# Optimization experiments

Hardware: AMD Instinct MI355X
Metric: run time of the kernel (lower is better)

## Reference

```python
import jax, jax.numpy as jnp
import numpy as np

NUM_NODES = 1_000_000
IN_F, HID_F, OUT_F = 128, 128, 128
N0, N1, T = 16384, 4096, 16


def _safediv(a, b):
    return a / jnp.where(b == 0, jnp.ones_like(b), b)


def _conv(h, nodeset, nb_nodes, nb_w, Qw, Qb, Ww, Wb):
    # gather self + neighbor embeddings (irregular access)
    h_self = h[nodeset]                                   # [n, in]
    h_nb = h[nb_nodes]                                    # [n, T, in]
    q = jax.nn.leaky_relu(jnp.einsum('nti,hi->nth', h_nb, Qw) + Qb)
    agg = _safediv((nb_w[:, :, None] * q).sum(1), nb_w.sum(1, keepdims=True))  # [n, hid]
    h_cat = jnp.concatenate([h_self, agg], axis=1)        # [n, in+hid]
    h_new = jax.nn.leaky_relu(h_cat @ Ww.T + Wb)          # [n, out]
    nrm = jnp.linalg.norm(h_new, axis=1, keepdims=True)
    return _safediv(h_new, nrm)


def setup_inputs() -> dict:
    key = jax.random.key(0)
    ks = jax.random.split(key, 16)
    xav = lambda k, o, i: jax.random.uniform(k, (o, i), jnp.float32, -1.0, 1.0) * jnp.sqrt(6.0 / (o + i)) * jnp.sqrt(2.0)
    return {
        'h': jax.random.normal(ks[0], (NUM_NODES, IN_F), jnp.float32),
        'Qw0': xav(ks[1], HID_F, IN_F), 'Qb0': jnp.zeros((HID_F,), jnp.float32),
        'Ww0': xav(ks[2], HID_F, IN_F + HID_F), 'Wb0': jnp.zeros((HID_F,), jnp.float32),
        'Qw1': xav(ks[3], OUT_F, HID_F), 'Qb1': jnp.zeros((OUT_F,), jnp.float32),
        'Ww1': xav(ks[4], OUT_F, HID_F + OUT_F), 'Wb1': jnp.zeros((OUT_F,), jnp.float32),
        'nodeset0': jax.random.randint(ks[5], (N0,), 0, NUM_NODES, jnp.int32),
        'nb_nodes0': jax.random.randint(ks[6], (N0, T), 0, NUM_NODES, jnp.int32),
        'nb_weights0': jax.random.uniform(ks[7], (N0, T), jnp.float32),
        'nodeset1': jax.random.randint(ks[8], (N1,), 0, NUM_NODES, jnp.int32),
        'nb_nodes1': jax.random.randint(ks[9], (N1, T), 0, NUM_NODES, jnp.int32),
        'nb_weights1': jax.random.uniform(ks[10], (N1, T), jnp.float32),
    }


def reference(h, Qw0, Qb0, Ww0, Wb0, Qw1, Qb1, Ww1, Wb1,
              nodeset0, nb_nodes0, nb_weights0,
              nodeset1, nb_nodes1, nb_weights1):
    # layer 0: conv then scatter back into embedding table
    new0 = _conv(h, nodeset0, nb_nodes0, nb_weights0, Qw0, Qb0, Ww0, Wb0)
    h = h.at[nodeset0].set(new0)
    # layer 1
    new1 = _conv(h, nodeset1, nb_nodes1, nb_weights1, Qw1, Qb1, Ww1, Wb1)
    h = h.at[nodeset1].set(new1)
    return h[nodeset1]  # [N1, OUT_F]
```

## Files before the change

### kernel.cpp

```cpp
#include <hip/hip_runtime.h>
#include <hip/hip_bf16.h>
#include <math.h>

#define NN 1000000
#define F 128
#define N0 16384
#define N1 4096

typedef __attribute__((ext_vector_type(8))) short bf16x8;
typedef __attribute__((ext_vector_type(4))) float f32x4;

__device__ inline unsigned short f2b(float f) {
    union { float f; unsigned u; } v; v.f = f;
    unsigned r = v.u + 0x7FFFu + ((v.u >> 16) & 1u);
    return (unsigned short)(r >> 16);
}

__device__ inline bf16x8 pack8(float4 a, float4 b) {
    union { __hip_bfloat162 h2[4]; bf16x8 v; } u;
    u.h2[0] = __float22bfloat162_rn(make_float2(a.x, a.y));
    u.h2[1] = __float22bfloat162_rn(make_float2(a.z, a.w));
    u.h2[2] = __float22bfloat162_rn(make_float2(b.x, b.y));
    u.h2[3] = __float22bfloat162_rn(make_float2(b.z, b.w));
    return u.v;
}


__global__ void k_prep(const int* __restrict__ ns0, const int* __restrict__ ns1,
                       int* __restrict__ map0, int* __restrict__ map1,
                       const float* __restrict__ Qw0, const float* __restrict__ Qw1,
                       const float* __restrict__ Ww0, const float* __restrict__ Ww1,
                       unsigned short* __restrict__ Qw0b, unsigned short* __restrict__ Qw1b,
                       unsigned short* __restrict__ Ww0b, unsigned short* __restrict__ Ww1b) {
    int i = blockIdx.x * blockDim.x + threadIdx.x;
    int nt = gridDim.x * blockDim.x;
    if (i < N0) atomicMax(&map0[ns0[i]], i);
    if (i < N1) atomicMax(&map1[ns1[i]], i);
    for (int j = i; j < 128 * 128; j += nt) { Qw0b[j] = f2b(Qw0[j]); Qw1b[j] = f2b(Qw1[j]); }
    for (int j = i; j < 128 * 256; j += nt) { Ww0b[j] = f2b(Ww0[j]); Ww1b[j] = f2b(Ww1[j]); }
}


__global__ __launch_bounds__(512, 4) void k_layer(
    const float* __restrict__ h, const unsigned short* __restrict__ newprevb,
    const int* __restrict__ mapprev,
    const int* __restrict__ nodeset, const int* __restrict__ nb,
    const float* __restrict__ nbw,
    const unsigned short* __restrict__ Qwb, const float* __restrict__ Qb,
    const unsigned short* __restrict__ Wwb, const float* __restrict__ Wb,
    float* __restrict__ outf, unsigned short* __restrict__ outb)
{
    __shared__ unsigned short lQ[128 * 128];
    __shared__ unsigned short lA[16 * 256];
    __shared__ float sred[8][16];
    const int tid = threadIdx.x;
    const int wid = tid >> 6, lane = tid & 63;
    const int row = lane & 15, kg = lane >> 4;
    const long mbase = (long)blockIdx.x * 16;

    float4 sv[4];
    uint4 sb[2];
    bool sredir = false;
    const int sq = tid & 7;
    if (tid < 128) {
        int sr = tid >> 3;
        int gs = nodeset[mbase + sr];
        int p = mapprev ? mapprev[gs] : -1;
        if (p >= 0) {
            sredir = true;
            const uint4* s = (const uint4*)(newprevb + (size_t)p * F + sq * 16);
            sb[0] = s[0]; sb[1] = s[1];
        } else {
            const float4* s = (const float4*)(h + (size_t)gs * F + sq * 16);
            sv[0] = s[0]; sv[1] = s[1]; sv[2] = s[2]; sv[3] = s[3];
        }
    }

    const long nodebase = mbase + wid * 2;
    float w[2][4];
#pragma unroll
    for (int nn = 0; nn < 2; ++nn)
#pragma unroll
        for (int r = 0; r < 4; ++r) w[nn][r] = nbw[(nodebase + nn) * 16 + kg * 4 + r];

    bf16x8 Ab[2][4];
    {
        float4 av[2][8];
        bool redir[2];
#pragma unroll
        for (int nn = 0; nn < 2; ++nn) {
            long node = nodebase + nn;
            int g = nb[node * 16 + row];
            int p = mapprev ? mapprev[g] : -1;
            redir[nn] = (p >= 0);
            if (p >= 0) {
                const bf16x8* s = (const bf16x8*)(newprevb + (size_t)p * F);
#pragma unroll
                for (int kk = 0; kk < 4; ++kk) Ab[nn][kk] = s[kk * 4 + kg];
            } else {
                const float4* s4 = (const float4*)(h + (size_t)g * F);
#pragma unroll
                for (int kk = 0; kk < 4; ++kk) {
                    av[nn][kk * 2]     = s4[kk * 8 + kg * 2];
                    av[nn][kk * 2 + 1] = s4[kk * 8 + kg * 2 + 1];
                }
            }
        }
#pragma unroll
        for (int nn = 0; nn < 2; ++nn)
            if (!redir[nn]) {
#pragma unroll
                for (int kk = 0; kk < 4; ++kk)
                    Ab[nn][kk] = pack8(av[nn][kk * 2], av[nn][kk * 2 + 1]);
            }
    }

    for (int c = tid; c < 2048; c += 512) {
        int j = c >> 4;
        uint4 v = ((const uint4*)Qwb)[c];
        *(uint4*)((char*)lQ + ((c << 4) ^ ((j & 7) << 4))) = v;
    }

    if (tid < 128) {
        int sr = tid >> 3;
        int b0 = sr * 512 + sq * 32;
        int swz = (sr & 7) << 4;
        if (sredir) {
            *(uint4*)((char*)lA + (b0 ^ swz)) = sb[0];
            *(uint4*)((char*)lA + ((b0 + 16) ^ swz)) = sb[1];
        } else {
            *(bf16x8*)((char*)lA + (b0 ^ swz)) = pack8(sv[0], sv[1]);
            *(bf16x8*)((char*)lA + ((b0 + 16) ^ swz)) = pack8(sv[2], sv[3]);
        }
    }
    __syncthreads();

    float inv[2];
#pragma unroll
    for (int nn = 0; nn < 2; ++nn) {
        float ws = w[nn][0] + w[nn][1] + w[nn][2] + w[nn][3];
        ws += __shfl_xor(ws, 16);
        ws += __shfl_xor(ws, 32);
        inv[nn] = (ws == 0.f) ? 1.f : 1.f / ws;
    }

#pragma unroll 1
    for (int half = 0; half < 2; ++half) {
        f32x4 acc[2][4];
#pragma unroll
        for (int nn = 0; nn < 2; ++nn)
#pragma unroll
            for (int jt = 0; jt < 4; ++jt)
                acc[nn][jt] = (f32x4){0.f, 0.f, 0.f, 0.f};

#pragma unroll
        for (int kk = 0; kk < 4; ++kk) {
            bf16x8 Bf[4];
#pragma unroll
            for (int jt = 0; jt < 4; ++jt) {
                int j = (half * 4 + jt) * 16 + row;
                int byte = ((j << 8) + (kk << 6) + (kg << 4)) ^ ((j & 7) << 4);
                Bf[jt] = *(bf16x8*)((char*)lQ + byte);
            }
#pragma unroll
            for (int jt = 0; jt < 4; ++jt) {
                acc[0][jt] = __builtin_amdgcn_mfma_f32_16x16x32_bf16(Ab[0][kk], Bf[jt], acc[0][jt], 0, 0, 0);
                acc[1][jt] = __builtin_amdgcn_mfma_f32_16x16x32_bf16(Ab[1][kk], Bf[jt], acc[1][jt], 0, 0, 0);
            }
        }

#pragma unroll
        for (int nn = 0; nn < 2; ++nn) {
            int nl = wid * 2 + nn;
#pragma unroll
            for (int jt = 0; jt < 4; ++jt) {
                int jtg = half * 4 + jt;
                float qb = Qb[jtg * 16 + row];
                float t = 0.f;
#pragma unroll
                for (int r = 0; r < 4; ++r) {
                    float v = acc[nn][jt][r] + qb;
                    v = v > 0.f ? v : 0.01f * v;
                    t = fmaf(w[nn][r], v, t);
                }
                t += __shfl_xor(t, 16);
                t += __shfl_xor(t, 32);
                if (lane < 16) {
                    int byte = (nl * 512 + 256 + jtg * 32 + lane * 2) ^ ((nl & 7) << 4);
                    *(unsigned short*)((char*)lA + byte) = f2b(t * inv[nn]);
                }
            }
        }
    }
    __syncthreads();

    const int j = wid * 16 + row;
    f32x4 dacc = (f32x4){0.f, 0.f, 0.f, 0.f};
#pragma unroll
    for (int kk = 0; kk < 8; ++kk) {
        bf16x8 a = *(bf16x8*)((char*)lA + ((row * 512 + kk * 64 + kg * 16) ^ ((row & 7) << 4)));
        bf16x8 b = ((const bf16x8*)(Wwb + (size_t)j * 256))[kk * 4 + kg];
        dacc = __builtin_amdgcn_mfma_f32_16x16x32_bf16(a, b, dacc, 0, 0, 0);
    }

    float wb = Wb[j];
    float ss[4];
#pragma unroll
    for (int r = 0; r < 4; ++r) {
        float v = dacc[r] + wb;
        v = v > 0.f ? v : 0.01f * v;
        dacc[r] = v;
        ss[r] = v * v;
    }
#pragma unroll
    for (int r = 0; r < 4; ++r) {
        ss[r] += __shfl_xor(ss[r], 1);
        ss[r] += __shfl_xor(ss[r], 2);
        ss[r] += __shfl_xor(ss[r], 4);
        ss[r] += __shfl_xor(ss[r], 8);
    }
    if (row == 0) {
#pragma unroll
        for (int r = 0; r < 4; ++r) sred[wid][kg * 4 + r] = ss[r];
    }
    __syncthreads();
    float invn[4];
#pragma unroll
    for (int r = 0; r < 4; ++r) {
        float s = 0.f;
#pragma unroll
        for (int w8 = 0; w8 < 8; ++w8) s += sred[w8][kg * 4 + r];
        float n = sqrtf(s);
        invn[r] = (n == 0.f) ? 1.f : 1.f / n;
    }
    if (outf) {
#pragma unroll
        for (int r = 0; r < 4; ++r)
            outf[(size_t)(mbase + kg * 4 + r) * F + j] = dacc[r] * invn[r];
    } else {
#pragma unroll
        for (int r = 0; r < 4; ++r)
            outb[(size_t)(mbase + kg * 4 + r) * F + j] = f2b(dacc[r] * invn[r]);
    }
}


__global__ void k_fix(const int* __restrict__ map1, const int* __restrict__ ns1,
                      float* __restrict__ out, int n) {
    int i = blockIdx.x * blockDim.x + threadIdx.x;
    if (i < n) {
        int p = map1[ns1[i]];
        if (p != i) {
            float4* o = (float4*)out;
#pragma unroll
            for (int c = 0; c < 32; ++c) o[(size_t)i * 32 + c] = o[(size_t)p * 32 + c];
        }
    }
}


extern "C" void kernel_launch(void* const* d_in, const int* in_sizes, int n_in,
                              void* d_out, int out_size, void* d_ws, size_t ws_size,
                              hipStream_t stream) {
    const float* h    = (const float*)d_in[0];
    const float* Qw0  = (const float*)d_in[1];
    const float* Qb0  = (const float*)d_in[2];
    const float* Ww0  = (const float*)d_in[3];
    const float* Wb0  = (const float*)d_in[4];
    const float* Qw1  = (const float*)d_in[5];
    const float* Qb1  = (const float*)d_in[6];
    const float* Ww1  = (const float*)d_in[7];
    const float* Wb1  = (const float*)d_in[8];
    const int*   ns0  = (const int*)d_in[9];
    const int*   nb0  = (const int*)d_in[10];
    const float* nbw0 = (const float*)d_in[11];
    const int*   ns1  = (const int*)d_in[12];
    const int*   nb1  = (const int*)d_in[13];
    const float* nbw1 = (const float*)d_in[14];

    int* map0 = (int*)d_ws;
    int* map1 = map0 + NN;
    unsigned short* new0b = (unsigned short*)(map1 + NN);
    unsigned short* Qw0b = new0b + (size_t)N0 * F;
    unsigned short* Qw1b = Qw0b + 128 * 128;
    unsigned short* Ww0b = Qw1b + 128 * 128;
    unsigned short* Ww1b = Ww0b + 128 * 256;

    hipMemsetAsync(map0, 0xFF, (size_t)2 * NN * sizeof(int), stream);
    k_prep<<<64, 256, 0, stream>>>(ns0, ns1, map0, map1,
                                   Qw0, Qw1, Ww0, Ww1, Qw0b, Qw1b, Ww0b, Ww1b);

    k_layer<<<N0 / 16, 512, 0, stream>>>(h, nullptr, nullptr, ns0, nb0, nbw0,
                                         Qw0b, Qb0, Ww0b, Wb0, nullptr, new0b);

    k_layer<<<N1 / 16, 512, 0, stream>>>(h, new0b, map0, ns1, nb1, nbw1,
                                         Qw1b, Qb1, Ww1b, Wb1, (float*)d_out, nullptr);

    k_fix<<<(N1 + 255) / 256, 256, 0, stream>>>(map1, ns1, (float*)d_out, N1);
}
```

Baseline: 79.08 us.

## Replace dense node maps with hash tables built inside layer-0 kernel

Drops the 8 MB memset of two dense million-entry index maps and uses small open-addressing hash tables (64K and 16K slots) instead. The tables are cleared in the prep kernel and filled by the first layer kernel, so the separate atomic build pass goes away. Layer 1 and the fix kernel look up redirects by probing the tables. The self-row gather also moves to 256 threads with narrower loads, and the neighbor-weight loads are reordered. The cost is probe loops with possible collisions and extra atomics inside layer 0.

```diff
diff --git a/kernel.cpp b/kernel.cpp
--- a/kernel.cpp
+++ b/kernel.cpp
@@ -6,6 +6,8 @@
 #define F 128
 #define N0 16384
 #define N1 4096
+#define HS0 65536
+#define HS1 16384
 
 typedef __attribute__((ext_vector_type(8))) short bf16x8;
 typedef __attribute__((ext_vector_type(4))) float f32x4;
@@ -26,16 +28,39 @@
 }
 
 
-__global__ void k_prep(const int* __restrict__ ns0, const int* __restrict__ ns1,
-                       int* __restrict__ map0, int* __restrict__ map1,
-                       const float* __restrict__ Qw0, const float* __restrict__ Qw1,
-                       const float* __restrict__ Ww0, const float* __restrict__ Ww1,
-                       unsigned short* __restrict__ Qw0b, unsigned short* __restrict__ Qw1b,
-                       unsigned short* __restrict__ Ww0b, unsigned short* __restrict__ Ww1b) {
+__device__ inline void hins(unsigned* __restrict__ keys, unsigned* __restrict__ vals,
+                            unsigned mask, unsigned g, unsigned pos1) {
+    unsigned s = (g * 2654435761u) & mask;
+    while (true) {
+        unsigned prev = atomicCAS(&keys[s], 0xFFFFFFFFu, g);
+        if (prev == 0xFFFFFFFFu || prev == g) { atomicMax(&vals[s], pos1); return; }
+        s = (s + 1) & mask;
+    }
+}
+
+__device__ inline int hfind(const unsigned* __restrict__ keys,
+                            const unsigned* __restrict__ vals,
+                            unsigned mask, unsigned g) {
+    unsigned s = (g * 2654435761u) & mask;
+    while (true) {
+        unsigned k = keys[s];
+        if (k == g) return (int)vals[s] - 1;
+        if (k == 0xFFFFFFFFu) return -1;
+        s = (s + 1) & mask;
+    }
+}
+
+
+__global__ void k_pre(unsigned* __restrict__ k0, unsigned* __restrict__ v0,
+                      unsigned* __restrict__ k1, unsigned* __restrict__ v1,
+                      const float* __restrict__ Qw0, const float* __restrict__ Qw1,
+                      const float* __restrict__ Ww0, const float* __restrict__ Ww1,
+                      unsigned short* __restrict__ Qw0b, unsigned short* __restrict__ Qw1b,
+                      unsigned short* __restrict__ Ww0b, unsigned short* __restrict__ Ww1b) {
     int i = blockIdx.x * blockDim.x + threadIdx.x;
     int nt = gridDim.x * blockDim.x;
-    if (i < N0) atomicMax(&map0[ns0[i]], i);
-    if (i < N1) atomicMax(&map1[ns1[i]], i);
+    for (int j = i; j < HS0; j += nt) { k0[j] = 0xFFFFFFFFu; v0[j] = 0u; }
+    for (int j = i; j < HS1; j += nt) { k1[j] = 0xFFFFFFFFu; v1[j] = 0u; }
     for (int j = i; j < 128 * 128; j += nt) { Qw0b[j] = f2b(Qw0[j]); Qw1b[j] = f2b(Qw1[j]); }
     for (int j = i; j < 128 * 256; j += nt) { Ww0b[j] = f2b(Ww0[j]); Ww1b[j] = f2b(Ww1[j]); }
 }
@@ -43,12 +68,14 @@
 
 __global__ __launch_bounds__(512, 4) void k_layer(
     const float* __restrict__ h, const unsigned short* __restrict__ newprevb,
-    const int* __restrict__ mapprev,
+    const unsigned* __restrict__ lk, const unsigned* __restrict__ lv, unsigned lmask,
     const int* __restrict__ nodeset, const int* __restrict__ nb,
     const float* __restrict__ nbw,
     const unsigned short* __restrict__ Qwb, const float* __restrict__ Qb,
     const unsigned short* __restrict__ Wwb, const float* __restrict__ Wb,
-    float* __restrict__ outf, unsigned short* __restrict__ outb)
+    float* __restrict__ outf, unsigned short* __restrict__ outb,
+    const int* __restrict__ ins0, unsigned* __restrict__ ik0, unsigned* __restrict__ iv0,
+    const int* __restrict__ ins1, unsigned* __restrict__ ik1, unsigned* __restrict__ iv1)
 {
     __shared__ unsigned short lQ[128 * 128];
     __shared__ unsigned short lA[16 * 256];
@@ -58,61 +85,64 @@
     const int row = lane & 15, kg = lane >> 4;
     const long mbase = (long)blockIdx.x * 16;
 
-    float4 sv[4];
-    uint4 sb[2];
+    if (ik0) {
+        int base = blockIdx.x * 16;
+        if (tid < 16) {
+            int i = base + tid;
+            if (i < N0) hins(ik0, iv0, HS0 - 1, (unsigned)ins0[i], (unsigned)(i + 1));
+        } else if (tid < 32) {
+            int i = base + tid - 16;
+            if (i < N1) hins(ik1, iv1, HS1 - 1, (unsigned)ins1[i], (unsigned)(i + 1));
+        }
+    }
+
+    const int sr = tid >> 4, sq = tid & 15;
+    const bool sact = tid < 256;
     bool sredir = false;
-    const int sq = tid & 7;
-    if (tid < 128) {
-        int sr = tid >> 3;
+    float4 sv0, sv1;
+    uint4 sb;
+    if (sact) {
         int gs = nodeset[mbase + sr];
-        int p = mapprev ? mapprev[gs] : -1;
+        int p = lk ? hfind(lk, lv, lmask, (unsigned)gs) : -1;
         if (p >= 0) {
             sredir = true;
-            const uint4* s = (const uint4*)(newprevb + (size_t)p * F + sq * 16);
-            sb[0] = s[0]; sb[1] = s[1];
+            sb = *(const uint4*)(newprevb + (size_t)p * F + sq * 8);
         } else {
-            const float4* s = (const float4*)(h + (size_t)gs * F + sq * 16);
-            sv[0] = s[0]; sv[1] = s[1]; sv[2] = s[2]; sv[3] = s[3];
+            const float4* s = (const float4*)(h + (size_t)gs * F) + sq * 2;
+            sv0 = s[0]; sv1 = s[1];
         }
     }
 
     const long nodebase = mbase + wid * 2;
-    float w[2][4];
-#pragma unroll
-    for (int nn = 0; nn < 2; ++nn)
-#pragma unroll
-        for (int r = 0; r < 4; ++r) w[nn][r] = nbw[(nodebase + nn) * 16 + kg * 4 + r];
-
+    int g0 = nb[nodebase * 16 + row];
+    int g1 = nb[(nodebase + 1) * 16 + row];
+    int p0 = lk ? hfind(lk, lv, lmask, (unsigned)g0) : -1;
+    int p1 = lk ? hfind(lk, lv, lmask, (unsigned)g1) : -1;
     bf16x8 Ab[2][4];
-    {
-        float4 av[2][8];
-        bool redir[2];
-#pragma unroll
-        for (int nn = 0; nn < 2; ++nn) {
-            long node = nodebase + nn;
-            int g = nb[node * 16 + row];
-            int p = mapprev ? mapprev[g] : -1;
-            redir[nn] = (p >= 0);
-            if (p >= 0) {
-                const bf16x8* s = (const bf16x8*)(newprevb + (size_t)p * F);
-#pragma unroll
-                for (int kk = 0; kk < 4; ++kk) Ab[nn][kk] = s[kk * 4 + kg];
-            } else {
-                const float4* s4 = (const float4*)(h + (size_t)g * F);
-#pragma unroll
-                for (int kk = 0; kk < 4; ++kk) {
-                    av[nn][kk * 2]     = s4[kk * 8 + kg * 2];
-                    av[nn][kk * 2 + 1] = s4[kk * 8 + kg * 2 + 1];
-                }
-            }
-        }
-#pragma unroll
-        for (int nn = 0; nn < 2; ++nn)
-            if (!redir[nn]) {
-#pragma unroll
-                for (int kk = 0; kk < 4; ++kk)
-                    Ab[nn][kk] = pack8(av[nn][kk * 2], av[nn][kk * 2 + 1]);
-            }
+    float4 av[2][8];
+    if (p0 >= 0) {
+        const bf16x8* s = (const bf16x8*)(newprevb + (size_t)p0 * F);
+#pragma unroll
+        for (int kk = 0; kk < 4; ++kk) Ab[0][kk] = s[kk * 4 + kg];
+    } else {
+        const float4* s4 = (const float4*)(h + (size_t)g0 * F);
+#pragma unroll
+        for (int kk = 0; kk < 4; ++kk) {
+            av[0][kk * 2]     = s4[kk * 8 + kg * 2];
+            av[0][kk * 2 + 1] = s4[kk * 8 + kg * 2 + 1];
+        }
+    }
+    if (p1 >= 0) {
+        const bf16x8* s = (const bf16x8*)(newprevb + (size_t)p1 * F);
+#pragma unroll
+        for (int kk = 0; kk < 4; ++kk) Ab[1][kk] = s[kk * 4 + kg];
+    } else {
+        const float4* s4 = (const float4*)(h + (size_t)g1 * F);
+#pragma unroll
+        for (int kk = 0; kk < 4; ++kk) {
+            av[1][kk * 2]     = s4[kk * 8 + kg * 2];
+            av[1][kk * 2 + 1] = s4[kk * 8 + kg * 2 + 1];
+        }
     }
 
     for (int c = tid; c < 2048; c += 512) {
@@ -121,17 +151,26 @@
         *(uint4*)((char*)lQ + ((c << 4) ^ ((j & 7) << 4))) = v;
     }
 
-    if (tid < 128) {
-        int sr = tid >> 3;
-        int b0 = sr * 512 + sq * 32;
+    float w[2][4];
+#pragma unroll
+    for (int nn = 0; nn < 2; ++nn)
+#pragma unroll
+        for (int r = 0; r < 4; ++r) w[nn][r] = nbw[(nodebase + nn) * 16 + kg * 4 + r];
+
+    if (p0 < 0) {
+#pragma unroll
+        for (int kk = 0; kk < 4; ++kk) Ab[0][kk] = pack8(av[0][kk * 2], av[0][kk * 2 + 1]);
+    }
+    if (p1 < 0) {
+#pragma unroll
+        for (int kk = 0; kk < 4; ++kk) Ab[1][kk] = pack8(av[1][kk * 2], av[1][kk * 2 + 1]);
+    }
+
+    if (sact) {
+        int b0 = sr * 512 + sq * 16;
         int swz = (sr & 7) << 4;
-        if (sredir) {
-            *(uint4*)((char*)lA + (b0 ^ swz)) = sb[0];
-            *(uint4*)((char*)lA + ((b0 + 16) ^ swz)) = sb[1];
-        } else {
-            *(bf16x8*)((char*)lA + (b0 ^ swz)) = pack8(sv[0], sv[1]);
-            *(bf16x8*)((char*)lA + ((b0 + 16) ^ swz)) = pack8(sv[2], sv[3]);
-        }
+        if (sredir) *(uint4*)((char*)lA + (b0 ^ swz)) = sb;
+        else        *(bf16x8*)((char*)lA + (b0 ^ swz)) = pack8(sv0, sv1);
     }
     __syncthreads();
 
@@ -245,11 +284,11 @@
 }
 
 
-__global__ void k_fix(const int* __restrict__ map1, const int* __restrict__ ns1,
-                      float* __restrict__ out, int n) {
+__global__ void k_fix(const unsigned* __restrict__ k1, const unsigned* __restrict__ v1,
+                      const int* __restrict__ ns1, float* __restrict__ out, int n) {
     int i = blockIdx.x * blockDim.x + threadIdx.x;
     if (i < n) {
-        int p = map1[ns1[i]];
+        int p = hfind(k1, v1, HS1 - 1, (unsigned)ns1[i]);
         if (p != i) {
             float4* o = (float4*)out;
 #pragma unroll
@@ -278,23 +317,28 @@
     const int*   nb1  = (const int*)d_in[13];
     const float* nbw1 = (const float*)d_in[14];
 
-    int* map0 = (int*)d_ws;
-    int* map1 = map0 + NN;
-    unsigned short* new0b = (unsigned short*)(map1 + NN);
+    unsigned* hk0 = (unsigned*)d_ws;
+    unsigned* hv0 = hk0 + HS0;
+    unsigned* hk1 = hv0 + HS0;
+    unsigned* hv1 = hk1 + HS1;
+    unsigned short* new0b = (unsigned short*)(hv1 + HS1);
     unsigned short* Qw0b = new0b + (size_t)N0 * F;
     unsigned short* Qw1b = Qw0b + 128 * 128;
     unsigned short* Ww0b = Qw1b + 128 * 128;
     unsigned short* Ww1b = Ww0b + 128 * 256;
 
-    hipMemsetAsync(map0, 0xFF, (size_t)2 * NN * sizeof(int), stream);
-    k_prep<<<64, 256, 0, stream>>>(ns0, ns1, map0, map1,
+    k_pre<<<128, 256, 0, stream>>>(hk0, hv0, hk1, hv1,
                                    Qw0, Qw1, Ww0, Ww1, Qw0b, Qw1b, Ww0b, Ww1b);
 
-    k_layer<<<N0 / 16, 512, 0, stream>>>(h, nullptr, nullptr, ns0, nb0, nbw0,
-                                         Qw0b, Qb0, Ww0b, Wb0, nullptr, new0b);
-
-    k_layer<<<N1 / 16, 512, 0, stream>>>(h, new0b, map0, ns1, nb1, nbw1,
-                                         Qw1b, Qb1, Ww1b, Wb1, (float*)d_out, nullptr);
-
-    k_fix<<<(N1 + 255) / 256, 256, 0, stream>>>(map1, ns1, (float*)d_out, N1);
-}
+    k_layer<<<N0 / 16, 512, 0, stream>>>(h, nullptr, nullptr, nullptr, 0u,
+                                         ns0, nb0, nbw0, Qw0b, Qb0, Ww0b, Wb0,
+                                         nullptr, new0b,
+                                         ns0, hk0, hv0, ns1, hk1, hv1);
+
+    k_layer<<<N1 / 16, 512, 0, stream>>>(h, new0b, hk0, hv0, HS0 - 1,
+                                         ns1, nb1, nbw1, Qw1b, Qb1, Ww1b, Wb1,
+                                         (float*)d_out, nullptr,
+                                         nullptr, nullptr, nullptr, nullptr, nullptr, nullptr);
+
+    k_fix<<<(N1 + 255) / 256, 256, 0, stream>>>(hk1, hv1, ns1, (float*)d_out, N1);
+}
```

Result: no change. 79.18 us (+0.1%).
